# Kernel optimization log

Hardware: AMD Instinct MI355X
Metric: run time of the kernel (lower is better)

Reference implementation:

```python
import jax, jax.numpy as jnp
import numpy as np

N_NODES = 100000
N_EDGES = 1600000
IN_DIM = 128
OUT_DIM = 64


def setup_inputs() -> dict:
    key = jax.random.key(0)
    k1, k2, k3 = jax.random.split(key, 3)
    x = jax.random.normal(k1, (N_NODES, IN_DIM), dtype=jnp.float32)
    edge_index = jax.random.randint(k2, (2, N_EDGES), 0, N_NODES, dtype=jnp.int64)
    W = jax.random.normal(k3, (IN_DIM, OUT_DIM), dtype=jnp.float32) * (1.0 / np.sqrt(IN_DIM))
    b = jnp.zeros((OUT_DIM,), dtype=jnp.float32)
    return {"x": x, "edge_index": edge_index, "W": W, "b": b}


def reference(x, edge_index, W, b):
    row = edge_index[0]  # source nodes
    col = edge_index[1]  # target nodes (aggregation index)
    n = x.shape[0]

    # gcn_norm with add_self_loops=False: degree from edge weights (ones) at target
    ones = jnp.ones((edge_index.shape[1],), dtype=x.dtype)
    deg = jax.ops.segment_sum(ones, col, num_segments=n)  # [N]
    deg_inv_sqrt = jnp.where(deg > 0, jax.lax.rsqrt(jnp.maximum(deg, 1e-12)), 0.0)
    norm = deg_inv_sqrt[row] * deg_inv_sqrt[col]  # [E]

    # linear transform first (bias added after aggregation, as in PyG GCNConv)
    h = x @ W  # [N, OUT_DIM]

    # gather source features, scale by norm, scatter-add to targets
    msg = h[row] * norm[:, None]  # [E, OUT_DIM]
    out = jax.ops.segment_sum(msg, col, num_segments=n) + b  # [N, OUT_DIM]

    return jax.nn.relu(out)
```

## Files before the change

### kernel.cpp

```cpp
#include <hip/hip_runtime.h>
#include <hip/hip_bf16.h>

#define IN_DIM 128
#define OUT_DIM 64
#define FLOG 7
#define FNPB (1 << FLOG)
#define MAXFINE 1024
#define BB 512
#define BT 512
#define MAXE 8
#define CAP 4096
#define SPILL_MAX 65536

static inline size_t align_up(size_t v, size_t a) { return (v + a - 1) & ~(a - 1); }

__device__ __forceinline__ unsigned short f2bf(float f) {
    unsigned int x = __float_as_uint(f);
    unsigned int r = (x + 0x7fffu + ((x >> 16) & 1u)) >> 16;
    return (unsigned short)r;
}

typedef _Float16 half8 __attribute__((ext_vector_type(8)));
typedef float f32x4 __attribute__((ext_vector_type(4)));

__global__ void __launch_bounds__(BT, 4) k_build_mm(
    const int* __restrict__ row, const int* __restrict__ col,
    int* __restrict__ BinSize, unsigned int* __restrict__ EdgeBuf,
    uint2* __restrict__ spill, int* __restrict__ spillcur,
    const float* __restrict__ x, const float* __restrict__ W,
    unsigned short* __restrict__ h,
    int n_edges, int n_nodes, int nbf, int chunk, int mm_blocks) {
    if ((int)blockIdx.x < BB) {
        __shared__ int hist[MAXFINE];
        int t = threadIdx.x;
        int start = blockIdx.x * chunk;
        int end = min(n_edges, start + chunk);
        int n = end - start;

        for (int i = t; i < nbf; i += BT) hist[i] = 0;
        __syncthreads();

        int er[MAXE], ec[MAXE];
#pragma unroll
        for (int u = 0; u < MAXE; ++u) {
            int i = t + u * BT;
            ec[u] = -1;
            if (i < n) {
                er[u] = row[start + i];
                int c = col[start + i];
                ec[u] = c;
                atomicAdd(&hist[c >> FLOG], 1);
            }
        }
        __syncthreads();
        for (int i = t; i < nbf; i += BT) {
            int cv = hist[i];
            hist[i] = cv ? atomicAdd(&BinSize[i], cv) : 0;
        }
        __syncthreads();
#pragma unroll
        for (int u = 0; u < MAXE; ++u) {
            int c = ec[u];
            if (c >= 0) {
                int bin = c >> FLOG;
                int pos = atomicAdd(&hist[bin], 1);
                if (pos < CAP) {
                    EdgeBuf[(size_t)bin * CAP + pos] =
                        ((unsigned int)er[u] << FLOG) | (unsigned int)(c & (FNPB - 1));
                } else {
                    int sp = atomicAdd(spillcur, 1);
                    if (sp < SPILL_MAX)
                        spill[sp] = make_uint2((unsigned int)er[u], (unsigned int)c);
                }
            }
        }
    } else {
        const int lane = threadIdx.x & 63;
        const int m = lane & 15;
        const int q = lane >> 4;
        const int wv = threadIdx.x >> 6;
        const int wid0 = ((int)blockIdx.x - BB) * 8 + wv;
        const int nwaves = mm_blocks * 8;
        const int ntiles = (n_nodes + 15) >> 4;

        half8 bfrag[4][4];
#pragma unroll
        for (int kt = 0; kt < 4; ++kt) {
#pragma unroll
            for (int nt = 0; nt < 4; ++nt) {
                int k0 = kt * 32 + q * 8;
                int c = nt * 16 + m;
#pragma unroll
                for (int j = 0; j < 8; ++j)
                    bfrag[kt][nt][j] = (_Float16)W[(size_t)(k0 + j) * OUT_DIM + c];
            }
        }

        for (int wid = wid0; wid < ntiles; wid += nwaves) {
            const int nb = wid << 4;
            int arow = nb + m;
            if (arow >= n_nodes) arow = n_nodes - 1;
            const float* xr = x + (size_t)arow * IN_DIM;

            f32x4 acc[4];
#pragma unroll
            for (int nt = 0; nt < 4; ++nt) acc[nt] = (f32x4){0.f, 0.f, 0.f, 0.f};

#pragma unroll
            for (int kt = 0; kt < 4; ++kt) {
                const float4* xp = (const float4*)(xr + kt * 32 + q * 8);
                float4 lo = xp[0];
                float4 hi = xp[1];
                half8 afrag;
                afrag[0] = (_Float16)lo.x; afrag[1] = (_Float16)lo.y;
                afrag[2] = (_Float16)lo.z; afrag[3] = (_Float16)lo.w;
                afrag[4] = (_Float16)hi.x; afrag[5] = (_Float16)hi.y;
                afrag[6] = (_Float16)hi.z; afrag[7] = (_Float16)hi.w;
#pragma unroll
                for (int nt = 0; nt < 4; ++nt)
                    acc[nt] = __builtin_amdgcn_mfma_f32_16x16x32_f16(
                        afrag, bfrag[kt][nt], acc[nt], 0, 0, 0);
            }

#pragma unroll
            for (int r = 0; r < 4; ++r) {
                int node = nb + q * 4 + r;
                if (node < n_nodes) {
                    unsigned short* hp = h + (size_t)node * OUT_DIM + m;
#pragma unroll
                    for (int nt = 0; nt < 4; ++nt)
                        hp[nt * 16] = f2bf(acc[nt][r]);
                }
            }
        }
    }
}

__global__ void __launch_bounds__(256) kD_degree(
    const unsigned int* __restrict__ EdgeBuf, const int* __restrict__ BinSize,
    const uint2* __restrict__ spill, const int* __restrict__ spillcur,
    float* __restrict__ dis, int n_nodes) {
    __shared__ int cnt[FNPB];
    int t = threadIdx.x;
    int b = blockIdx.x;
    if (t < FNPB) cnt[t] = 0;
    __syncthreads();
    int sz = min(BinSize[b], CAP);
    const unsigned int* slot = EdgeBuf + (size_t)b * CAP;
    for (int i = t; i < sz; i += 256)
        atomicAdd(&cnt[slot[i] & (FNPB - 1)], 1);
    int sn = min(*spillcur, SPILL_MAX);
    for (int i = t; i < sn; i += 256) {
        uint2 e = spill[i];
        if ((int)(e.y >> FLOG) == b) atomicAdd(&cnt[e.y & (FNPB - 1)], 1);
    }
    __syncthreads();
    int node = (b << FLOG) + t;
    if (t < FNPB && node < n_nodes) {
        int d = cnt[t];
        dis[node] = (d > 0) ? rsqrtf((float)d) : 0.0f;
    }
}

__global__ void __launch_bounds__(512) kF_sortagg(
    const unsigned int* __restrict__ EdgeBuf, const int* __restrict__ BinSize,
    const uint2* __restrict__ spill, const int* __restrict__ spillcur,
    const unsigned short* __restrict__ h, const float* __restrict__ dis,
    const float* __restrict__ b,
    float* __restrict__ out, int* __restrict__ arena, int* __restrict__ arenacur,
    int n_nodes) {
    __shared__ int cnt[FNPB];
    __shared__ int seg[FNPB];
    __shared__ int cursor[FNPB];
    __shared__ int sbuf[CAP];
    __shared__ int abase_sh;
    int t = threadIdx.x;
    int bk = blockIdx.x;
    int nb0 = bk << FLOG;
    int sz = min(BinSize[bk], CAP);
    const unsigned int* slot = EdgeBuf + (size_t)bk * CAP;
    int sn = min(*spillcur, SPILL_MAX);

    if (t < FNPB) cnt[t] = 0;
    __syncthreads();
    for (int i = t; i < sz; i += 512)
        atomicAdd(&cnt[slot[i] & (FNPB - 1)], 1);
    for (int i = t; i < sn; i += 512) {
        uint2 e = spill[i];
        if ((int)(e.y >> FLOG) == bk) atomicAdd(&cnt[e.y & (FNPB - 1)], 1);
    }
    __syncthreads();

    if (t < FNPB) seg[t] = cnt[t];
    __syncthreads();
    for (int off = 1; off < FNPB; off <<= 1) {
        int x = 0;
        if (t < FNPB && t >= off) x = seg[t - off];
        __syncthreads();
        if (t < FNPB) seg[t] += x;
        __syncthreads();
    }
    if (t < FNPB) cursor[t] = seg[t] - cnt[t];
    __syncthreads();

    int ne = seg[FNPB - 1];
    if (t == 0 && ne > CAP) abase_sh = atomicAdd(arenacur, ne);
    __syncthreads();

    const int lane = t & 63;
    const int wv = t >> 6;
    const int quarter = lane >> 4;
    const int qlane = lane & 15;
    float4 bias = ((const float4*)b)[qlane];

    if (ne <= CAP) {
        for (int i = t; i < sz; i += 512) {
            unsigned int v = slot[i];
            int p = atomicAdd(&cursor[v & (FNPB - 1)], 1);
            sbuf[p] = (int)(v >> FLOG);
        }
        for (int i = t; i < sn; i += 512) {
            uint2 e = spill[i];
            if ((int)(e.y >> FLOG) == bk) {
                int p = atomicAdd(&cursor[e.y & (FNPB - 1)], 1);
                sbuf[p] = (int)e.x;
            }
        }
        __syncthreads();

        for (int nl = wv; nl < FNPB; nl += 8) {
            int node = nb0 + nl;
            if (node >= n_nodes) break;
            int e_ = seg[nl];
            int dcount = cnt[nl];
            int s_ = e_ - dcount;
            float a0 = 0.f, a1 = 0.f, a2 = 0.f, a3 = 0.f;
            for (int j0 = s_; j0 < e_; j0 += 8) {
                int iA = j0 + quarter;
                int iB = j0 + quarter + 4;
                int rA = sbuf[iA < e_ ? iA : s_];
                int rB = sbuf[iB < e_ ? iB : s_];
                float dA = dis[rA];
                float dB = dis[rB];
                uint2 vA = make_uint2(0u, 0u), vB = make_uint2(0u, 0u);
                if (iA < e_)
                    vA = *(const uint2*)(h + (size_t)rA * OUT_DIM + qlane * 4);
                if (iB < e_)
                    vB = *(const uint2*)(h + (size_t)rB * OUT_DIM + qlane * 4);
                a0 = fmaf(__uint_as_float(vA.x << 16), dA, a0);
                a1 = fmaf(__uint_as_float(vA.x & 0xFFFF0000u), dA, a1);
                a2 = fmaf(__uint_as_float(vA.y << 16), dA, a2);
                a3 = fmaf(__uint_as_float(vA.y & 0xFFFF0000u), dA, a3);
                a0 = fmaf(__uint_as_float(vB.x << 16), dB, a0);
                a1 = fmaf(__uint_as_float(vB.x & 0xFFFF0000u), dB, a1);
                a2 = fmaf(__uint_as_float(vB.y << 16), dB, a2);
                a3 = fmaf(__uint_as_float(vB.y & 0xFFFF0000u), dB, a3);
            }
            a0 += __shfl_xor(a0, 16, 64); a0 += __shfl_xor(a0, 32, 64);
            a1 += __shfl_xor(a1, 16, 64); a1 += __shfl_xor(a1, 32, 64);
            a2 += __shfl_xor(a2, 16, 64); a2 += __shfl_xor(a2, 32, 64);
            a3 += __shfl_xor(a3, 16, 64); a3 += __shfl_xor(a3, 32, 64);
            if (quarter == 0) {
                float dv = (dcount > 0) ? rsqrtf((float)dcount) : 0.0f;
                float4 o;
                o.x = fmaxf(fmaf(a0, dv, bias.x), 0.f);
                o.y = fmaxf(fmaf(a1, dv, bias.y), 0.f);
                o.z = fmaxf(fmaf(a2, dv, bias.z), 0.f);
                o.w = fmaxf(fmaf(a3, dv, bias.w), 0.f);
                ((float4*)(out + (size_t)node * OUT_DIM))[qlane] = o;
            }
        }
    } else {
        int abase = abase_sh;
        for (int i = t; i < sz; i += 512) {
            unsigned int v = slot[i];
            int p = atomicAdd(&cursor[v & (FNPB - 1)], 1);
            arena[abase + p] = (int)(v >> FLOG);
        }
        for (int i = t; i < sn; i += 512) {
            uint2 e = spill[i];
            if ((int)(e.y >> FLOG) == bk) {
                int p = atomicAdd(&cursor[e.y & (FNPB - 1)], 1);
                arena[abase + p] = (int)e.x;
            }
        }
        __threadfence();
        __syncthreads();
        for (int nl = wv; nl < FNPB; nl += 8) {
            int node = nb0 + nl;
            if (node >= n_nodes) break;
            int e_ = seg[nl];
            int dcount = cnt[nl];
            int s_ = e_ - dcount;
            float a0 = 0.f, a1 = 0.f, a2 = 0.f, a3 = 0.f;
            for (int j0 = s_; j0 < e_; j0 += 8) {
                int iA = j0 + quarter;
                int iB = j0 + quarter + 4;
                int rA = arena[abase + (iA < e_ ? iA : s_)];
                int rB = arena[abase + (iB < e_ ? iB : s_)];
                float dA = dis[rA];
                float dB = dis[rB];
                uint2 vA = make_uint2(0u, 0u), vB = make_uint2(0u, 0u);
                if (iA < e_)
                    vA = *(const uint2*)(h + (size_t)rA * OUT_DIM + qlane * 4);
                if (iB < e_)
                    vB = *(const uint2*)(h + (size_t)rB * OUT_DIM + qlane * 4);
                a0 = fmaf(__uint_as_float(vA.x << 16), dA, a0);
                a1 = fmaf(__uint_as_float(vA.x & 0xFFFF0000u), dA, a1);
                a2 = fmaf(__uint_as_float(vA.y << 16), dA, a2);
                a3 = fmaf(__uint_as_float(vA.y & 0xFFFF0000u), dA, a3);
                a0 = fmaf(__uint_as_float(vB.x << 16), dB, a0);
                a1 = fmaf(__uint_as_float(vB.x & 0xFFFF0000u), dB, a1);
                a2 = fmaf(__uint_as_float(vB.y << 16), dB, a2);
                a3 = fmaf(__uint_as_float(vB.y & 0xFFFF0000u), dB, a3);
            }
            a0 += __shfl_xor(a0, 16, 64); a0 += __shfl_xor(a0, 32, 64);
            a1 += __shfl_xor(a1, 16, 64); a1 += __shfl_xor(a1, 32, 64);
            a2 += __shfl_xor(a2, 16, 64); a2 += __shfl_xor(a2, 32, 64);
            a3 += __shfl_xor(a3, 16, 64); a3 += __shfl_xor(a3, 32, 64);
            if (quarter == 0) {
                float dv = (dcount > 0) ? rsqrtf((float)dcount) : 0.0f;
                float4 o;
                o.x = fmaxf(fmaf(a0, dv, bias.x), 0.f);
                o.y = fmaxf(fmaf(a1, dv, bias.y), 0.f);
                o.z = fmaxf(fmaf(a2, dv, bias.z), 0.f);
                o.w = fmaxf(fmaf(a3, dv, bias.w), 0.f);
                ((float4*)(out + (size_t)node * OUT_DIM))[qlane] = o;
            }
        }
    }
}

#define MM_NODES 16
__global__ void __launch_bounds__(256) k_matmul_f32(
    const float* __restrict__ x, const float* __restrict__ W,
    const float* __restrict__ dis, float* __restrict__ h, int n_nodes) {
    __shared__ float xs[MM_NODES * IN_DIM];
    const int lane = threadIdx.x & 63;
    const int wv = threadIdx.x >> 6;
    float w[IN_DIM];
#pragma unroll
    for (int k = 0; k < IN_DIM; ++k) w[k] = W[k * OUT_DIM + lane];
    int nchunks = (n_nodes + MM_NODES - 1) / MM_NODES;
    for (int ch = blockIdx.x; ch < nchunks; ch += gridDim.x) {
        int base = ch * MM_NODES;
        int nrows = min(MM_NODES, n_nodes - base);
        __syncthreads();
        const float4* xg = (const float4*)(x + (size_t)base * IN_DIM);
        int nf4 = nrows * IN_DIM / 4;
        for (int i = threadIdx.x; i < nf4; i += 256) ((float4*)xs)[i] = xg[i];
        __syncthreads();
#pragma unroll
        for (int j = 0; j < 4; ++j) {
            int local = wv * 4 + j;
            int node = base + local;
            if (local < nrows) {
                const float4* xr = (const float4*)(xs + local * IN_DIM);
                float acc = 0.0f;
#pragma unroll
                for (int k4 = 0; k4 < IN_DIM / 4; ++k4) {
                    float4 xv = xr[k4];
                    acc = fmaf(xv.x, w[k4 * 4 + 0], acc);
                    acc = fmaf(xv.y, w[k4 * 4 + 1], acc);
                    acc = fmaf(xv.z, w[k4 * 4 + 2], acc);
                    acc = fmaf(xv.w, w[k4 * 4 + 3], acc);
                }
                h[(size_t)node * OUT_DIM + lane] = acc * dis[node];
            }
        }
    }
}

__global__ void k_degree_fb(const int* __restrict__ col, int* __restrict__ deg,
                            int n_edges) {
    int i = blockIdx.x * blockDim.x + threadIdx.x;
    int stride = gridDim.x * blockDim.x;
    for (; i < n_edges; i += stride) atomicAdd(&deg[col[i]], 1);
}

__global__ void k_rsqrt_fb(const int* __restrict__ deg, float* __restrict__ dis, int n) {
    int i = blockIdx.x * blockDim.x + threadIdx.x;
    if (i < n) {
        int d = deg[i];
        dis[i] = (d > 0) ? rsqrtf((float)d) : 0.0f;
    }
}

__global__ void __launch_bounds__(256) k_scatter_fb(
    const int* __restrict__ row, const int* __restrict__ col,
    const float* __restrict__ dis, const float* __restrict__ h,
    float* __restrict__ out, int n_edges) {
    const int lane = threadIdx.x & 63;
    int e = (blockIdx.x * blockDim.x + threadIdx.x) >> 6;
    int nw = (gridDim.x * blockDim.x) >> 6;
    for (; e < n_edges; e += nw) {
        int r = row[e];
        int c = col[e];
        float v = h[(size_t)r * OUT_DIM + lane] * dis[c];
        atomicAdd(&out[(size_t)c * OUT_DIM + lane], v);
    }
}

__global__ void k_bias_relu_fb(float* __restrict__ out, const float* __restrict__ b,
                               int total) {
    int i = blockIdx.x * blockDim.x + threadIdx.x;
    int stride = gridDim.x * blockDim.x;
    for (; i < total; i += stride) {
        float v = out[i] + b[i & (OUT_DIM - 1)];
        out[i] = fmaxf(v, 0.0f);
    }
}

extern "C" void kernel_launch(void* const* d_in, const int* in_sizes, int n_in,
                              void* d_out, int out_size, void* d_ws, size_t ws_size,
                              hipStream_t stream) {
    const float* x = (const float*)d_in[0];
    const int* ei = (const int*)d_in[1];
    const float* W = (const float*)d_in[2];
    const float* b = (const float*)d_in[3];
    float* out = (float*)d_out;

    const int n_nodes = in_sizes[0] / IN_DIM;
    const int n_edges = in_sizes[1] / 2;
    const int* row = ei;
    const int* col = ei + n_edges;

    const int nbf = (n_nodes + FNPB - 1) >> FLOG;
    const int chunk = (n_edges + BB - 1) / BB;

    char* wsb = (char*)d_ws;
    size_t off = 0;
    int* BinSize = (int*)(wsb + off);    off += (size_t)(nbf + 8) * 4;
    int* spillcur = BinSize + nbf;
    int* arenacur = BinSize + nbf + 1;
    const size_t zero_bytes = off;
    off = align_up(off, 256);
    unsigned int* EdgeBuf = (unsigned int*)(wsb + off);
                                         off += align_up((size_t)nbf * CAP * 4, 256);
    uint2* spill = (uint2*)(wsb + off);  off += align_up((size_t)SPILL_MAX * 8, 256);
    int* arena = (int*)(wsb + off);      off += align_up((size_t)n_edges * 4, 256);
    float* dis = (float*)(wsb + off);    off += align_up((size_t)n_nodes * 4, 256);
    unsigned short* h = (unsigned short*)(wsb + off);
                                         off += (size_t)n_nodes * OUT_DIM * 2;
    const size_t needed = off;

    const bool ok = (ws_size >= needed) && (nbf <= MAXFINE) &&
                    (chunk <= MAXE * BT) && (n_nodes <= (1 << 24));

    if (ok) {
        const int ntiles = (n_nodes + 15) >> 4;
        int mm_blocks = (ntiles + 15) / 16;
        if (mm_blocks < 1) mm_blocks = 1;
        hipMemsetAsync(BinSize, 0, zero_bytes, stream);
        k_build_mm<<<BB + mm_blocks, BT, 0, stream>>>(
            row, col, BinSize, EdgeBuf, spill, spillcur,
            x, W, h, n_edges, n_nodes, nbf, chunk, mm_blocks);
        kD_degree<<<nbf, 256, 0, stream>>>(EdgeBuf, BinSize, spill, spillcur,
                                           dis, n_nodes);
        kF_sortagg<<<nbf, 512, 0, stream>>>(EdgeBuf, BinSize, spill, spillcur,
                                            h, dis, b, out, arena, arenacur,
                                            n_nodes);
    } else {
        char* p = (char*)d_ws;
        int* deg_f = (int*)p;
        float* dis_f = (float*)(p + align_up((size_t)n_nodes * 4, 256));
        float* h_f = (float*)(p + 2 * align_up((size_t)n_nodes * 4, 256));
        hipMemsetAsync(deg_f, 0, (size_t)n_nodes * 4, stream);
        hipMemsetAsync(out, 0, (size_t)out_size * 4, stream);
        k_degree_fb<<<1024, 256, 0, stream>>>(col, deg_f, n_edges);
        k_rsqrt_fb<<<(n_nodes + 255) / 256, 256, 0, stream>>>(deg_f, dis_f, n_nodes);
        k_matmul_f32<<<1024, 256, 0, stream>>>(x, W, dis_f, h_f, n_nodes);
        k_scatter_fb<<<2048, 256, 0, stream>>>(row, col, dis_f, h_f, out, n_edges);
        k_bias_relu_fb<<<2048, 256, 0, stream>>>(out, b, n_nodes * OUT_DIM);
    }
}
```

Measured before the change: 181.4 us.

## Fold degree count into build kernel with global atomics, drop degree kernel

Removes the separate per-bin degree kernel: the binning pass now also does a global atomicAdd into a per-node degree array, and the aggregation kernel computes rsqrt of the degree on the fly for each gathered source. The binning blocks drop from 512 to 128 and use strided loops instead of register-cached edges, so row/col are re-read from global memory in the second pass. This saves one launch and one pass over EdgeBuf, at the cost of 1.6M global atomics, extra rsqrt work per edge, and fewer binning blocks working in parallel.

```diff
diff --git a/kernel.cpp b/kernel.cpp
--- a/kernel.cpp
+++ b/kernel.cpp
@@ -6,9 +6,8 @@
 #define FLOG 7
 #define FNPB (1 << FLOG)
 #define MAXFINE 1024
-#define BB 512
+#define BB 128
 #define BT 512
-#define MAXE 8
 #define CAP 4096
 #define SPILL_MAX 65536
 
@@ -27,6 +26,7 @@
     const int* __restrict__ row, const int* __restrict__ col,
     int* __restrict__ BinSize, unsigned int* __restrict__ EdgeBuf,
     uint2* __restrict__ spill, int* __restrict__ spillcur,
+    int* __restrict__ deg,
     const float* __restrict__ x, const float* __restrict__ W,
     unsigned short* __restrict__ h,
     int n_edges, int n_nodes, int nbf, int chunk, int mm_blocks) {
@@ -35,22 +35,14 @@
         int t = threadIdx.x;
         int start = blockIdx.x * chunk;
         int end = min(n_edges, start + chunk);
-        int n = end - start;
 
         for (int i = t; i < nbf; i += BT) hist[i] = 0;
         __syncthreads();
 
-        int er[MAXE], ec[MAXE];
-#pragma unroll
-        for (int u = 0; u < MAXE; ++u) {
-            int i = t + u * BT;
-            ec[u] = -1;
-            if (i < n) {
-                er[u] = row[start + i];
-                int c = col[start + i];
-                ec[u] = c;
-                atomicAdd(&hist[c >> FLOG], 1);
-            }
+        for (int i = start + t; i < end; i += BT) {
+            int c = col[i];
+            atomicAdd(&hist[c >> FLOG], 1);
+            atomicAdd(&deg[c], 1);
         }
         __syncthreads();
         for (int i = t; i < nbf; i += BT) {
@@ -58,20 +50,19 @@
             hist[i] = cv ? atomicAdd(&BinSize[i], cv) : 0;
         }
         __syncthreads();
-#pragma unroll
-        for (int u = 0; u < MAXE; ++u) {
-            int c = ec[u];
-            if (c >= 0) {
-                int bin = c >> FLOG;
-                int pos = atomicAdd(&hist[bin], 1);
-                if (pos < CAP) {
-                    EdgeBuf[(size_t)bin * CAP + pos] =
-                        ((unsigned int)er[u] << FLOG) | (unsigned int)(c & (FNPB - 1));
-                } else {
-                    int sp = atomicAdd(spillcur, 1);
-                    if (sp < SPILL_MAX)
-                        spill[sp] = make_uint2((unsigned int)er[u], (unsigned int)c);
-                }
+
+        for (int i = start + t; i < end; i += BT) {
+            int r = row[i];
+            int c = col[i];
+            int bin = c >> FLOG;
+            int pos = atomicAdd(&hist[bin], 1);
+            if (pos < CAP) {
+                EdgeBuf[(size_t)bin * CAP + pos] =
+                    ((unsigned int)r << FLOG) | (unsigned int)(c & (FNPB - 1));
+            } else {
+                int sp = atomicAdd(spillcur, 1);
+                if (sp < SPILL_MAX)
+                    spill[sp] = make_uint2((unsigned int)r, (unsigned int)c);
             }
         }
     } else {
@@ -136,36 +127,10 @@
     }
 }
 
-__global__ void __launch_bounds__(256) kD_degree(
-    const unsigned int* __restrict__ EdgeBuf, const int* __restrict__ BinSize,
-    const uint2* __restrict__ spill, const int* __restrict__ spillcur,
-    float* __restrict__ dis, int n_nodes) {
-    __shared__ int cnt[FNPB];
-    int t = threadIdx.x;
-    int b = blockIdx.x;
-    if (t < FNPB) cnt[t] = 0;
-    __syncthreads();
-    int sz = min(BinSize[b], CAP);
-    const unsigned int* slot = EdgeBuf + (size_t)b * CAP;
-    for (int i = t; i < sz; i += 256)
-        atomicAdd(&cnt[slot[i] & (FNPB - 1)], 1);
-    int sn = min(*spillcur, SPILL_MAX);
-    for (int i = t; i < sn; i += 256) {
-        uint2 e = spill[i];
-        if ((int)(e.y >> FLOG) == b) atomicAdd(&cnt[e.y & (FNPB - 1)], 1);
-    }
-    __syncthreads();
-    int node = (b << FLOG) + t;
-    if (t < FNPB && node < n_nodes) {
-        int d = cnt[t];
-        dis[node] = (d > 0) ? rsqrtf((float)d) : 0.0f;
-    }
-}
-
 __global__ void __launch_bounds__(512) kF_sortagg(
     const unsigned int* __restrict__ EdgeBuf, const int* __restrict__ BinSize,
     const uint2* __restrict__ spill, const int* __restrict__ spillcur,
-    const unsigned short* __restrict__ h, const float* __restrict__ dis,
+    const unsigned short* __restrict__ h, const int* __restrict__ deg,
     const float* __restrict__ b,
     float* __restrict__ out, int* __restrict__ arena, int* __restrict__ arenacur,
     int n_nodes) {
@@ -240,8 +205,10 @@
                 int iB = j0 + quarter + 4;
                 int rA = sbuf[iA < e_ ? iA : s_];
                 int rB = sbuf[iB < e_ ? iB : s_];
-                float dA = dis[rA];
-                float dB = dis[rB];
+                int dAi = deg[rA];
+                int dBi = deg[rB];
+                float dA = (dAi > 0) ? rsqrtf((float)dAi) : 0.0f;
+                float dB = (dBi > 0) ? rsqrtf((float)dBi) : 0.0f;
                 uint2 vA = make_uint2(0u, 0u), vB = make_uint2(0u, 0u);
                 if (iA < e_)
                     vA = *(const uint2*)(h + (size_t)rA * OUT_DIM + qlane * 4);
@@ -298,8 +265,10 @@
                 int iB = j0 + quarter + 4;
                 int rA = arena[abase + (iA < e_ ? iA : s_)];
                 int rB = arena[abase + (iB < e_ ? iB : s_)];
-                float dA = dis[rA];
-                float dB = dis[rB];
+                int dAi = deg[rA];
+                int dBi = deg[rB];
+                float dA = (dAi > 0) ? rsqrtf((float)dAi) : 0.0f;
+                float dB = (dBi > 0) ? rsqrtf((float)dBi) : 0.0f;
                 uint2 vA = make_uint2(0u, 0u), vB = make_uint2(0u, 0u);
                 if (iA < e_)
                     vA = *(const uint2*)(h + (size_t)rA * OUT_DIM + qlane * 4);
@@ -433,19 +402,20 @@
     int* BinSize = (int*)(wsb + off);    off += (size_t)(nbf + 8) * 4;
     int* spillcur = BinSize + nbf;
     int* arenacur = BinSize + nbf + 1;
+    off = align_up(off, 256);
+    int* deg = (int*)(wsb + off);        off += (size_t)n_nodes * 4;
     const size_t zero_bytes = off;
     off = align_up(off, 256);
     unsigned int* EdgeBuf = (unsigned int*)(wsb + off);
                                          off += align_up((size_t)nbf * CAP * 4, 256);
     uint2* spill = (uint2*)(wsb + off);  off += align_up((size_t)SPILL_MAX * 8, 256);
     int* arena = (int*)(wsb + off);      off += align_up((size_t)n_edges * 4, 256);
-    float* dis = (float*)(wsb + off);    off += align_up((size_t)n_nodes * 4, 256);
     unsigned short* h = (unsigned short*)(wsb + off);
                                          off += (size_t)n_nodes * OUT_DIM * 2;
     const size_t needed = off;
 
     const bool ok = (ws_size >= needed) && (nbf <= MAXFINE) &&
-                    (chunk <= MAXE * BT) && (n_nodes <= (1 << 24));
+                    (n_nodes <= (1 << 24));
 
     if (ok) {
         const int ntiles = (n_nodes + 15) >> 4;
@@ -453,12 +423,10 @@
         if (mm_blocks < 1) mm_blocks = 1;
         hipMemsetAsync(BinSize, 0, zero_bytes, stream);
         k_build_mm<<<BB + mm_blocks, BT, 0, stream>>>(
-            row, col, BinSize, EdgeBuf, spill, spillcur,
+            row, col, BinSize, EdgeBuf, spill, spillcur, deg,
             x, W, h, n_edges, n_nodes, nbf, chunk, mm_blocks);
-        kD_degree<<<nbf, 256, 0, stream>>>(EdgeBuf, BinSize, spill, spillcur,
-                                           dis, n_nodes);
         kF_sortagg<<<nbf, 512, 0, stream>>>(EdgeBuf, BinSize, spill, spillcur,
-                                            h, dis, b, out, arena, arenacur,
+                                            h, deg, b, out, arena, arenacur,
                                             n_nodes);
     } else {
         char* p = (char*)d_ws;
```

Measured after the change: 229.8 us. 1.27x slower.
